# Kernel optimization log

Hardware: AMD Instinct MI355X
Metric: run time of the kernel (lower is better)

The kernel has to match this reference:

```python
import jax, jax.numpy as jnp
import numpy as np

# --- configuration matching setup_inputs ---
N_EVENTS = 4          # number of events in the ragged batch (row_splits has 5 entries)
HITS_PER_EVENT = 50000
K_CLUSTERS = 256      # max truth shower index per event
Q_MIN = 1.0
REPULSION_CONTRIB = 0.5
SCALE = 1.0
EPS = 1e-6


def setup_inputs() -> dict:
    key = jax.random.key(0)
    k1, k2 = jax.random.split(key)
    n = N_EVENTS * HITS_PER_EVENT
    coords = jax.random.normal(k1, (n, 3), dtype=jnp.float32)
    truth_indices = jax.random.randint(k2, (n, 1), 0, K_CLUSTERS, dtype=jnp.int32)
    row_splits = (jnp.arange(N_EVENTS + 1, dtype=jnp.int32) * HITS_PER_EVENT)
    return {"coords": coords, "truth_indices": truth_indices, "row_splits": row_splits}


def _oc_cluster_loss(coords, truth_indices):
    """Object-condensation attractive/repulsive potentials.

    coords:        [n, C] float clustering coordinates (n = E * Nev, equal splits)
    truth_indices: [n, 1] int cluster id per hit, in [0, K)
    Returns (V_att, V_rep) scalars, averaged over events.
    """
    C = coords.shape[1]
    x = coords.reshape(N_EVENTS, HITS_PER_EVENT, C)            # [E, N, C]
    t = truth_indices.reshape(N_EVENTS, HITS_PER_EVENT)        # [E, N]

    # beta_like = 0.5 (3-input path of LLClusterCoordinates) -> constant charge
    beta = jnp.float32(0.5)
    q_val = jnp.arctanh(beta) ** 2 + jnp.float32(Q_MIN)        # scalar
    q = jnp.full((N_EVENTS, HITS_PER_EVENT), q_val, dtype=coords.dtype)  # [E, N]

    # membership mask (one-hot over truth clusters)
    M = jax.nn.one_hot(t, K_CLUSTERS, dtype=coords.dtype)      # [E, N, K]
    qM = M * q[..., None]                                      # [E, N, K]

    # q-weighted average condensation point per cluster (use_average_cc_pos=True)
    sum_q = jnp.sum(qM, axis=1)                                # [E, K]
    x_cc = jnp.einsum('enk,enc->ekc', qM, x) / (sum_q[..., None] + EPS)  # [E, K, C]

    # charge of the condensation (max-beta) vertex per cluster
    q_alpha = jnp.max(qM, axis=1)                              # [E, K] (0 for empty clusters)

    # pairwise hit <-> condensation-point distances
    diff = x[:, :, None, :] - x_cc[:, None, :, :]              # [E, N, K, C]
    d2 = jnp.sum(diff * diff, axis=-1)                         # [E, N, K]
    d = jnp.sqrt(d2 + EPS)

    w = q[..., None] * q_alpha[:, None, :]                     # [E, N, K]
    n_per_ev = jnp.float32(HITS_PER_EVENT)

    V_att_ev = jnp.sum(M * w * d2, axis=(1, 2)) / n_per_ev                   # [E]
    V_rep_ev = jnp.sum((1.0 - M) * w * jax.nn.relu(1.0 - d), axis=(1, 2)) / n_per_ev
    return jnp.mean(V_att_ev), jnp.mean(V_rep_ev)


def reference(coords, truth_indices, row_splits):
    V_att, V_rep = _oc_cluster_loss(coords, truth_indices)
    lossval = SCALE * ((1.0 - REPULSION_CONTRIB) * V_att + REPULSION_CONTRIB * V_rep)
    # layer returns (inputs[0], lossval) when return_lossval=True
    return coords, lossval
```

## Files before the change

kernel.cpp:

```cpp
#include <hip/hip_runtime.h>

#define E_EVENTS 4
#define NPE 50000
#define K_CL 256
#define QV 1.30173724f
#define EPSF 1e-6f
#define SB 64
#define BPE 196
#define HALFK 128
#define LOSS_SCALE 2.5e-6f

__global__ __launch_bounds__(256) void k_sums(const float* __restrict__ coords,
                                              const int* __restrict__ truth,
                                              float* __restrict__ sums) {
    __shared__ float s[4 * K_CL];
    int tid = threadIdx.x;
    #pragma unroll
    for (int i = 0; i < 4; ++i) s[tid + 256 * i] = 0.0f;
    __syncthreads();

    int e = blockIdx.x / SB, blk = blockIdx.x % SB;
    for (int local = blk * 256 + tid; local < NPE; local += SB * 256) {
        int h = e * NPE + local;
        int t = truth[h];
        float x = coords[3 * h], y = coords[3 * h + 1], z = coords[3 * h + 2];
        atomicAdd(&s[t], x);
        atomicAdd(&s[K_CL + t], y);
        atomicAdd(&s[2 * K_CL + t], z);
        atomicAdd(&s[3 * K_CL + t], 1.0f);
    }
    __syncthreads();

    float cx = s[tid], cy = s[K_CL + tid], cz = s[2 * K_CL + tid], cn = s[3 * K_CL + tid];
    if (cn != 0.0f) {
        float* g = sums + ((e * K_CL + tid) << 2);
        atomicAdd(g + 0, cx);
        atomicAdd(g + 1, cy);
        atomicAdd(g + 2, cz);
        atomicAdd(g + 3, cn);
    }
}

__global__ void k_cc(const float* __restrict__ sums, float4* __restrict__ cc) {
    int i = blockIdx.x * blockDim.x + threadIdx.x;
    float sx = sums[4 * i], sy = sums[4 * i + 1], sz = sums[4 * i + 2], cn = sums[4 * i + 3];
    float inv = QV / (QV * cn + EPSF);
    float qa = (cn > 0.0f) ? QV : 0.0f;
    cc[i] = make_float4(sx * inv, sy * inv, sz * inv, qa);
}

__global__ __launch_bounds__(256) void k_main(const float* __restrict__ coords,
                                              const int* __restrict__ truth,
                                              const float4* __restrict__ cc,
                                              float* __restrict__ out) {
    __shared__ float4 scc[HALFK];
    int tid = threadIdx.x;
    int b = blockIdx.x;
    int e = b / (2 * BPE);
    int r = b - e * (2 * BPE);
    int hh = r / BPE;
    int blk = r - hh * BPE;
    if (tid < HALFK) scc[tid] = cc[e * K_CL + hh * HALFK + tid];
    __syncthreads();

    int local = blk * 256 + tid;
    float contrib = 0.0f;
    if (local < NPE) {
        int h = e * NPE + local;
        float x = coords[3 * h], y = coords[3 * h + 1], z = coords[3 * h + 2];
        int t = truth[h];
        if (hh == 0) {
            out[3 * h] = x; out[3 * h + 1] = y; out[3 * h + 2] = z;
        }

        float rep = 0.0f;
        #pragma unroll 8
        for (int k = 0; k < HALFK; ++k) {
            float4 c = scc[k];
            float dx = x - c.x, dy = y - c.y, dz = z - c.z;
            float d2e = fmaf(dx, dx, fmaf(dy, dy, fmaf(dz, dz, EPSF)));
            float d = __builtin_amdgcn_sqrtf(d2e);
            rep = fmaf(c.w, fmaxf(0.0f, 1.0f - d), rep);
        }
        contrib = QV * rep;
        if ((t >> 7) == hh) {
            float4 ct = scc[t & (HALFK - 1)];
            float dx = x - ct.x, dy = y - ct.y, dz = z - ct.z;
            float d2o = fmaf(dx, dx, fmaf(dy, dy, dz * dz));
            float dno = __builtin_amdgcn_sqrtf(d2o + EPSF);
            contrib += QV * fmaf(QV, d2o, -ct.w * fmaxf(0.0f, 1.0f - dno));
        }
    }

    #pragma unroll
    for (int o = 32; o > 0; o >>= 1) contrib += __shfl_down(contrib, o, 64);
    __shared__ float wsum[4];
    if ((tid & 63) == 0) wsum[tid >> 6] = contrib;
    __syncthreads();
    if (tid == 0) {
        float bsum = wsum[0] + wsum[1] + wsum[2] + wsum[3];
        atomicAdd(out + 3 * E_EVENTS * NPE, bsum * LOSS_SCALE);
    }
}

extern "C" void kernel_launch(void* const* d_in, const int* in_sizes, int n_in,
                              void* d_out, int out_size, void* d_ws, size_t ws_size,
                              hipStream_t stream) {
    const float* coords = (const float*)d_in[0];
    const int*   truth  = (const int*)d_in[1];

    float*  sums = (float*)d_ws;
    float4* cc   = (float4*)((char*)d_ws + 16384);
    float*  out  = (float*)d_out;

    hipMemsetAsync(d_ws, 0, 16384, stream);
    hipMemsetAsync(out + 3 * E_EVENTS * NPE, 0, 4, stream);

    k_sums<<<E_EVENTS * SB, 256, 0, stream>>>(coords, truth, sums);
    k_cc  <<<E_EVENTS * K_CL / 256, 256, 0, stream>>>(sums, cc);
    k_main<<<E_EVENTS * 2 * BPE, 256, 0, stream>>>(coords, truth, cc, out);
}
```

Before: 101.3 us.

## Replace global atomics and memsets with partial-sum reduction, pack repulsion loop

k_sums now writes per-block partial cluster sums to the workspace instead of doing global atomics. k_cc reduces those partials and zeroes the loss slot, so both hipMemsetAsync calls go away. The main kernel stores cluster centres as separate x/y/z/w arrays in shared memory and processes two clusters per iteration with 2-wide float vectors, aiming for packed FP32 math. This removes two memset launches and atomic contention, at the cost of a 1 MB partial buffer and a serial 64-way reduction inside k_cc.

```diff
diff --git a/kernel.cpp b/kernel.cpp
--- a/kernel.cpp
+++ b/kernel.cpp
@@ -1,4 +1,6 @@
 #include <hip/hip_runtime.h>
+
+typedef float v2f __attribute__((ext_vector_type(2)));
 
 #define E_EVENTS 4
 #define NPE 50000
@@ -9,17 +11,18 @@
 #define BPE 196
 #define HALFK 128
 #define LOSS_SCALE 2.5e-6f
+#define LOSS_IDX (3 * E_EVENTS * NPE)
 
 __global__ __launch_bounds__(256) void k_sums(const float* __restrict__ coords,
                                               const int* __restrict__ truth,
-                                              float* __restrict__ sums) {
+                                              float* __restrict__ partial) {
     __shared__ float s[4 * K_CL];
     int tid = threadIdx.x;
     #pragma unroll
     for (int i = 0; i < 4; ++i) s[tid + 256 * i] = 0.0f;
     __syncthreads();
 
-    int e = blockIdx.x / SB, blk = blockIdx.x % SB;
+    int e = blockIdx.x >> 6, blk = blockIdx.x & (SB - 1);
     for (int local = blk * 256 + tid; local < NPE; local += SB * 256) {
         int h = e * NPE + local;
         int t = truth[h];
@@ -31,36 +34,45 @@
     }
     __syncthreads();
 
-    float cx = s[tid], cy = s[K_CL + tid], cz = s[2 * K_CL + tid], cn = s[3 * K_CL + tid];
-    if (cn != 0.0f) {
-        float* g = sums + ((e * K_CL + tid) << 2);
-        atomicAdd(g + 0, cx);
-        atomicAdd(g + 1, cy);
-        atomicAdd(g + 2, cz);
-        atomicAdd(g + 3, cn);
-    }
+    float* g = partial + blockIdx.x * 1024;
+    #pragma unroll
+    for (int i = 0; i < 4; ++i) g[tid + 256 * i] = s[tid + 256 * i];
 }
 
-__global__ void k_cc(const float* __restrict__ sums, float4* __restrict__ cc) {
-    int i = blockIdx.x * blockDim.x + threadIdx.x;
-    float sx = sums[4 * i], sy = sums[4 * i + 1], sz = sums[4 * i + 2], cn = sums[4 * i + 3];
+__global__ __launch_bounds__(64) void k_cc(const float* __restrict__ partial,
+                                           float4* __restrict__ cc,
+                                           float* __restrict__ out) {
+    int gid = blockIdx.x * 64 + threadIdx.x;
+    int e = gid >> 8, k = gid & (K_CL - 1);
+    float sx = 0.f, sy = 0.f, sz = 0.f, cn = 0.f;
+    const float* base = partial + e * SB * 1024 + k;
+    #pragma unroll 4
+    for (int b = 0; b < SB; ++b) {
+        const float* p = base + b * 1024;
+        sx += p[0]; sy += p[256]; sz += p[512]; cn += p[768];
+    }
     float inv = QV / (QV * cn + EPSF);
     float qa = (cn > 0.0f) ? QV : 0.0f;
-    cc[i] = make_float4(sx * inv, sy * inv, sz * inv, qa);
+    cc[gid] = make_float4(sx * inv, sy * inv, sz * inv, qa);
+    if (gid == 0) out[LOSS_IDX] = 0.0f;
 }
 
 __global__ __launch_bounds__(256) void k_main(const float* __restrict__ coords,
                                               const int* __restrict__ truth,
                                               const float4* __restrict__ cc,
                                               float* __restrict__ out) {
-    __shared__ float4 scc[HALFK];
+    __shared__ v2f sxv[HALFK / 2], syv[HALFK / 2], szv[HALFK / 2], swv[HALFK / 2];
     int tid = threadIdx.x;
     int b = blockIdx.x;
     int e = b / (2 * BPE);
     int r = b - e * (2 * BPE);
     int hh = r / BPE;
     int blk = r - hh * BPE;
-    if (tid < HALFK) scc[tid] = cc[e * K_CL + hh * HALFK + tid];
+    if (tid < HALFK) {
+        float4 c = cc[e * K_CL + hh * HALFK + tid];
+        ((float*)sxv)[tid] = c.x; ((float*)syv)[tid] = c.y;
+        ((float*)szv)[tid] = c.z; ((float*)swv)[tid] = c.w;
+    }
     __syncthreads();
 
     int local = blk * 256 + tid;
@@ -73,22 +85,29 @@
             out[3 * h] = x; out[3 * h + 1] = y; out[3 * h + 2] = z;
         }
 
-        float rep = 0.0f;
+        const v2f ONE = {1.0f, 1.0f}, ZER = {0.0f, 0.0f}, EPS2 = {EPSF, EPSF};
+        v2f X = {x, x}, Y = {y, y}, Z = {z, z};
+        v2f rep = {0.0f, 0.0f};
         #pragma unroll 8
-        for (int k = 0; k < HALFK; ++k) {
-            float4 c = scc[k];
-            float dx = x - c.x, dy = y - c.y, dz = z - c.z;
-            float d2e = fmaf(dx, dx, fmaf(dy, dy, fmaf(dz, dz, EPSF)));
-            float d = __builtin_amdgcn_sqrtf(d2e);
-            rep = fmaf(c.w, fmaxf(0.0f, 1.0f - d), rep);
+        for (int k2 = 0; k2 < HALFK / 2; ++k2) {
+            v2f dx = X - sxv[k2], dy = Y - syv[k2], dz = Z - szv[k2];
+            v2f d2 = __builtin_elementwise_fma(dx, dx,
+                     __builtin_elementwise_fma(dy, dy,
+                     __builtin_elementwise_fma(dz, dz, EPS2)));
+            v2f d = {__builtin_amdgcn_sqrtf(d2.x), __builtin_amdgcn_sqrtf(d2.y)};
+            v2f rr = __builtin_elementwise_max(ONE - d, ZER);
+            rep = __builtin_elementwise_fma(swv[k2], rr, rep);
         }
-        contrib = QV * rep;
+        contrib = QV * (rep.x + rep.y);
+
         if ((t >> 7) == hh) {
-            float4 ct = scc[t & (HALFK - 1)];
-            float dx = x - ct.x, dy = y - ct.y, dz = z - ct.z;
+            int tl = t & (HALFK - 1);
+            float cx = ((float*)sxv)[tl], cy = ((float*)syv)[tl];
+            float cz = ((float*)szv)[tl], cw = ((float*)swv)[tl];
+            float dx = x - cx, dy = y - cy, dz = z - cz;
             float d2o = fmaf(dx, dx, fmaf(dy, dy, dz * dz));
             float dno = __builtin_amdgcn_sqrtf(d2o + EPSF);
-            contrib += QV * fmaf(QV, d2o, -ct.w * fmaxf(0.0f, 1.0f - dno));
+            contrib += QV * fmaf(QV, d2o, -cw * fmaxf(0.0f, 1.0f - dno));
         }
     }
 
@@ -99,7 +118,7 @@
     __syncthreads();
     if (tid == 0) {
         float bsum = wsum[0] + wsum[1] + wsum[2] + wsum[3];
-        atomicAdd(out + 3 * E_EVENTS * NPE, bsum * LOSS_SCALE);
+        atomicAdd(out + LOSS_IDX, bsum * LOSS_SCALE);
     }
 }
 
@@ -109,14 +128,11 @@
     const float* coords = (const float*)d_in[0];
     const int*   truth  = (const int*)d_in[1];
 
-    float*  sums = (float*)d_ws;
-    float4* cc   = (float4*)((char*)d_ws + 16384);
-    float*  out  = (float*)d_out;
+    float*  partial = (float*)d_ws;
+    float4* cc      = (float4*)((char*)d_ws + (1 << 20));
+    float*  out     = (float*)d_out;
 
-    hipMemsetAsync(d_ws, 0, 16384, stream);
-    hipMemsetAsync(out + 3 * E_EVENTS * NPE, 0, 4, stream);
-
-    k_sums<<<E_EVENTS * SB, 256, 0, stream>>>(coords, truth, sums);
-    k_cc  <<<E_EVENTS * K_CL / 256, 256, 0, stream>>>(sums, cc);
+    k_sums<<<E_EVENTS * SB, 256, 0, stream>>>(coords, truth, partial);
+    k_cc  <<<16, 64, 0, stream>>>(partial, cc, out);
     k_main<<<E_EVENTS * 2 * BPE, 256, 0, stream>>>(coords, truth, cc, out);
 }
```

New measurement: 98.74 us. -2.5%, faster.
